# Kernel optimization log

Measured on AMD Instinct MI355X. Metric: run time of the kernel, lower is better.

## Reference

```python
import jax, jax.numpy as jnp
import numpy as np

HIDDEN = 2048
HEAD_DIM = 128
NUM_HEADS = 8
NUM_HH = 2          # num_householder
CONV = 4
EPS = 1e-5
KEY_DIM = NUM_HEADS * HEAD_DIM  # 1024


def setup_inputs() -> dict:
    key = jax.random.key(0)
    ks = jax.random.split(key, 14)
    B, L = 2, 512
    s = 0.02
    x = jax.random.normal(ks[0], (B, L, HIDDEN), jnp.float32)
    Wq = jax.random.normal(ks[1], (HIDDEN, KEY_DIM), jnp.float32) * s
    Wk = jax.random.normal(ks[2], (HIDDEN, KEY_DIM * NUM_HH), jnp.float32) * s
    Wv = jax.random.normal(ks[3], (HIDDEN, KEY_DIM * NUM_HH), jnp.float32) * s
    Wb = jax.random.normal(ks[4], (HIDDEN, NUM_HEADS * NUM_HH), jnp.float32) * s
    Wa = jax.random.normal(ks[5], (HIDDEN, NUM_HEADS), jnp.float32) * s
    A_log = jnp.log(jax.random.uniform(ks[6], (NUM_HEADS,), jnp.float32, 1e-3, 16.0))
    dt = jnp.exp(jax.random.uniform(ks[7], (NUM_HEADS,), jnp.float32)
                 * (np.float32(np.log(0.1)) - np.float32(np.log(0.001)))
                 + np.float32(np.log(0.001)))
    dt = jnp.maximum(dt, 1e-4)
    dt_bias = dt + jnp.log(-jnp.expm1(-dt))
    conv_q_w = jax.random.normal(ks[8], (KEY_DIM, 1, CONV), jnp.float32) * 0.1
    conv_k_w = jax.random.normal(ks[9], (KEY_DIM * NUM_HH, 1, CONV), jnp.float32) * 0.1
    conv_v_w = jax.random.normal(ks[10], (KEY_DIM * NUM_HH, 1, CONV), jnp.float32) * 0.1
    Wg = jax.random.normal(ks[11], (HIDDEN, KEY_DIM), jnp.float32) * s
    norm_w = jnp.ones((HEAD_DIM,), jnp.float32)
    Wo = jax.random.normal(ks[12], (KEY_DIM, HIDDEN), jnp.float32) * s
    return dict(x=x, Wq=Wq, Wk=Wk, Wv=Wv, Wb=Wb, Wa=Wa, A_log=A_log,
                dt_bias=dt_bias, conv_q_w=conv_q_w, conv_k_w=conv_k_w,
                conv_v_w=conv_v_w, Wg=Wg, norm_w=norm_w, Wo=Wo)


def _causal_conv_silu(x, w):
    # x: (B, L, C); w: (C, 1, K) depthwise causal conv, then SiLU
    y = jax.lax.conv_general_dilated(
        jnp.swapaxes(x, 1, 2), w, window_strides=(1,),
        padding=[(w.shape[-1] - 1, 0)],
        feature_group_count=w.shape[0],
        dimension_numbers=('NCH', 'OIH', 'NCH'))
    return jnp.swapaxes(jax.nn.silu(y), 1, 2)


def _l2norm(x):
    n = jnp.sqrt(jnp.sum(x * x, axis=-1, keepdims=True))
    return x / jnp.maximum(n, 1e-12)


def reference(x, Wq, Wk, Wv, Wb, Wa, A_log, dt_bias,
              conv_q_w, conv_k_w, conv_v_w, Wg, norm_w, Wo):
    B, L, _ = x.shape
    H, Dh, nh = NUM_HEADS, HEAD_DIM, NUM_HH

    q = _causal_conv_silu(x @ Wq, conv_q_w).reshape(B, L, H, Dh)
    k = _causal_conv_silu(x @ Wk, conv_k_w).reshape(B, L, nh, H, Dh)
    v = _causal_conv_silu(x @ Wv, conv_v_w).reshape(B, L, nh, H, Dh)

    q = _l2norm(q) / np.float32(np.sqrt(Dh))
    k = _l2norm(k)

    beta = 2.0 * jax.nn.sigmoid(x @ Wb).reshape(B, L, nh, H)  # allow_neg_eigval
    g = -jnp.exp(A_log) * jax.nn.softplus(x @ Wa + dt_bias)    # (B, L, H)

    def step(state, inp):
        # state: (B, H, Dh, Dh)
        q_t, k_t, v_t, b_t, g_t = inp  # (B,H,Dh),(B,nh,H,Dh),(B,nh,H,Dh),(B,nh,H),(B,H)
        state = state * jnp.exp(g_t)[..., None, None]  # gate at first sub-step
        for j in range(nh):  # Householder / delta-rule updates
            kj = k_t[:, j]
            corr = jnp.einsum('bhk,bhkv->bhv', kj, state)
            u = (v_t[:, j] - corr) * b_t[:, j][..., None]
            state = state + jnp.einsum('bhk,bhv->bhkv', kj, u)
        o_t = jnp.einsum('bhk,bhkv->bhv', q_t, state)  # readout at last sub-step
        return state, o_t

    state0 = jnp.zeros((B, H, Dh, Dh), x.dtype)
    xs = (jnp.moveaxis(q, 1, 0), jnp.moveaxis(k, 1, 0), jnp.moveaxis(v, 1, 0),
          jnp.moveaxis(beta, 1, 0), jnp.moveaxis(g, 1, 0))
    state, o = jax.lax.scan(step, state0, xs)
    o = jnp.moveaxis(o, 0, 1)  # (B, L, H, Dh)

    # gated RMSNorm: normalize o, scale by weight, gate with silu(g_proj(x))
    gate = (x @ Wg).reshape(B, L, H, Dh)
    o = o * jax.lax.rsqrt(jnp.mean(o * o, axis=-1, keepdims=True) + EPS)
    o = o * norm_w * jax.nn.silu(gate)

    out = o.reshape(B, L, H * Dh) @ Wo
    return out, state
```

## Files before the change

### kernel.cpp

```cpp
#include <hip/hip_runtime.h>
#include <hip/hip_bf16.h>
#include <cmath>

#define B_   2
#define L_   512
#define HID  2048
#define DH   128
#define NH   8
#define NHH  2
#define ROWS 1024
#define NFUSE 6144

typedef float  f32x2  __attribute__((ext_vector_type(2)));
typedef float  f32x4  __attribute__((ext_vector_type(4)));
typedef __bf16 bf16x8 __attribute__((ext_vector_type(8)));

#define AS1(p) ((const __attribute__((address_space(1))) unsigned int*)(p))
#define AS3(p) ((__attribute__((address_space(3))) unsigned int*)(p))

__device__ __forceinline__ float dpp_xor1(float x) {
  int r = __builtin_amdgcn_update_dpp(0, __float_as_int(x), 0xB1, 0xF, 0xF, true);
  return __int_as_float(r);
}
__device__ __forceinline__ float dpp_xor2(float x) {
  int r = __builtin_amdgcn_update_dpp(0, __float_as_int(x), 0x4E, 0xF, 0xF, true);
  return __int_as_float(r);
}
__device__ __forceinline__ float dpp_hmirror(float x) {
  int r = __builtin_amdgcn_update_dpp(0, __float_as_int(x), 0x141, 0xF, 0xF, true);
  return __int_as_float(r);
}
__device__ __forceinline__ float dpp_rmirror(float x) {
  int r = __builtin_amdgcn_update_dpp(0, __float_as_int(x), 0x140, 0xF, 0xF, true);
  return __int_as_float(r);
}

__global__ void f2bf_kernel(const float* __restrict__ in, __hip_bfloat16* __restrict__ out, int n) {
  int i = blockIdx.x * 256 + threadIdx.x;
  if (i < n) out[i] = __float2bfloat16(in[i]);
}

__global__ __launch_bounds__(256) void transpose5_kernel(const float* __restrict__ Wq,
                                                         const float* __restrict__ Wk,
                                                         const float* __restrict__ Wv,
                                                         const float* __restrict__ Wg,
                                                         const float* __restrict__ Wo,
                                                         __hip_bfloat16* __restrict__ WT,
                                                         __hip_bfloat16* __restrict__ WoT) {
  const float* in; __hip_bfloat16* out; int K, N;
  switch (blockIdx.z) {
    case 0: in = Wq; out = WT;                          K = 2048; N = 1024; break;
    case 1: in = Wk; out = WT + (size_t)1024 * 2048;    K = 2048; N = 2048; break;
    case 2: in = Wv; out = WT + (size_t)3072 * 2048;    K = 2048; N = 2048; break;
    case 3: in = Wg; out = WT + (size_t)5120 * 2048;    K = 2048; N = 1024; break;
    default: in = Wo; out = WoT;                        K = 1024; N = 2048; break;
  }
  __shared__ float tile[32][33];
  int n0 = blockIdx.x * 32, k0 = blockIdx.y * 32;
  if (n0 >= N || k0 >= K) return;
  int tx = threadIdx.x, ty = threadIdx.y;
#pragma unroll
  for (int i = 0; i < 32; i += 8)
    tile[ty + i][tx] = in[(size_t)(k0 + ty + i) * N + n0 + tx];
  __syncthreads();
#pragma unroll
  for (int i = 0; i < 32; i += 8)
    out[(size_t)(n0 + ty + i) * K + k0 + tx] = __float2bfloat16(tile[tx][ty + i]);
}

__global__ __launch_bounds__(256) void gemm_bf16_64(const __hip_bfloat16* __restrict__ A,
                                                    const __hip_bfloat16* __restrict__ BT,
                                                    float* __restrict__ C, int M, int N, int K) {
  __shared__ __align__(16) __hip_bfloat16 lA[64 * 32];
  __shared__ __align__(16) __hip_bfloat16 lB[128 * 32];
  const int tid = threadIdx.x;
  const int lane = tid & 63;
  const int w = tid >> 6;
  const int row0 = blockIdx.y * 64;
  const int col0 = blockIdx.x * 128;
  f32x4 acc[4][2];
#pragma unroll
  for (int m = 0; m < 4; ++m)
#pragma unroll
    for (int n = 0; n < 2; ++n) acc[m][n] = {0.f, 0.f, 0.f, 0.f};
  const int fr = lane & 15;
  const int ko = (lane >> 4) * 8;
  for (int kt = 0; kt < K; kt += 32) {
    {
      int elem = (w * 64 + lane) * 8;
      int rr = elem >> 5, cc = elem & 31;
      const __hip_bfloat16* srcA = A + (size_t)(row0 + rr) * K + kt + cc;
      __builtin_amdgcn_global_load_lds(AS1(srcA), AS3(&lA[w * 512]), 16, 0, 0);
    }
#pragma unroll
    for (int i = 0; i < 2; ++i) {
      int elem = ((i * 4 + w) * 64 + lane) * 8;
      int rr = elem >> 5, cc = elem & 31;
      const __hip_bfloat16* srcB = BT + (size_t)(col0 + rr) * K + kt + cc;
      __builtin_amdgcn_global_load_lds(AS1(srcB), AS3(&lB[(i * 4 + w) * 512]), 16, 0, 0);
    }
    __syncthreads();
    bf16x8 af[4], bfr[2];
#pragma unroll
    for (int m = 0; m < 4; ++m)
      af[m] = *reinterpret_cast<const bf16x8*>(&lA[(m * 16 + fr) * 32 + ko]);
#pragma unroll
    for (int n = 0; n < 2; ++n)
      bfr[n] = *reinterpret_cast<const bf16x8*>(&lB[(w * 32 + n * 16 + fr) * 32 + ko]);
#pragma unroll
    for (int m = 0; m < 4; ++m)
#pragma unroll
      for (int n = 0; n < 2; ++n)
        acc[m][n] = __builtin_amdgcn_mfma_f32_16x16x32_bf16(af[m], bfr[n], acc[m][n], 0, 0, 0);
    __syncthreads();
  }
  const int rq = (lane >> 4) * 4;
#pragma unroll
  for (int m = 0; m < 4; ++m)
#pragma unroll
    for (int n = 0; n < 2; ++n)
#pragma unroll
      for (int r = 0; r < 4; ++r)
        C[(size_t)(row0 + m * 16 + rq + r) * N + (col0 + w * 32 + n * 16 + fr)] =
            acc[m][n][r];
}

__device__ __forceinline__ float silu_f(float y) { return y / (1.f + __expf(-y)); }

__global__ __launch_bounds__(64) void ba_fused_kernel(const float* __restrict__ x,
                                                      const float* __restrict__ Wb,
                                                      const float* __restrict__ Wa,
                                                      const float* __restrict__ A_log,
                                                      const float* __restrict__ dt_bias,
                                                      float* __restrict__ beta_s,
                                                      float* __restrict__ ge_s) {
  const int row = blockIdx.x;
  const int lane = threadIdx.x;
  f32x4 aB0 = {0,0,0,0}, aB1 = {0,0,0,0}, aB2 = {0,0,0,0}, aB3 = {0,0,0,0};
  f32x4 aA0 = {0,0,0,0}, aA1 = {0,0,0,0};
  const float* xr = x + (size_t)row * HID;
  for (int i = 0; i < 32; ++i) {
    int k = lane + i * 64;
    float xv = xr[k];
    const f32x4* wb4 = (const f32x4*)(Wb + (size_t)k * 16);
    const f32x4* wa4 = (const f32x4*)(Wa + (size_t)k * 8);
    aB0 += wb4[0] * xv; aB1 += wb4[1] * xv; aB2 += wb4[2] * xv; aB3 += wb4[3] * xv;
    aA0 += wa4[0] * xv; aA1 += wa4[1] * xv;
  }
  __shared__ float red[64][25];
#pragma unroll
  for (int c = 0; c < 4; ++c) {
    red[lane][0 + c]  = aB0[c];
    red[lane][4 + c]  = aB1[c];
    red[lane][8 + c]  = aB2[c];
    red[lane][12 + c] = aB3[c];
    red[lane][16 + c] = aA0[c];
    red[lane][20 + c] = aA1[c];
  }
  if (lane < 24) {
    float s = 0.f;
#pragma unroll 8
    for (int i = 0; i < 64; ++i) s += red[i][lane];
    int b = row >> 9, t = row & 511;
    if (lane < 16) {
      int j = lane >> 3, h = lane & 7;
      beta_s[(((size_t)(b * 8 + h)) * 2 + j) * 512 + t] = 2.f / (1.f + __expf(-s));
    } else {
      int h = lane - 16;
      float vv = s + dt_bias[h];
      float sp = (vv > 20.f) ? vv : log1pf(__expf(vv));
      ge_s[((size_t)(b * 8 + h)) * 512 + t] = __expf(-__expf(A_log[h]) * sp);
    }
  }
}

__global__ __launch_bounds__(128) void conv_qkv_kernel(const float* __restrict__ qkvg,
                                                       const float* __restrict__ wq,
                                                       const float* __restrict__ wk,
                                                       const float* __restrict__ wv,
                                                       float* __restrict__ q_s,
                                                       float* __restrict__ k_s,
                                                       float* __restrict__ v_s) {
  int bt = blockIdx.x;
  int yy = blockIdx.y;
  int d  = threadIdx.x;
  int b = bt >> 9, t = bt & 511;
  __shared__ float red[2];
  if (yy < 8) {
    int h = yy, c = h * 128 + d;
    float y = 0.f;
#pragma unroll
    for (int tau = 0; tau < 4; ++tau) {
      int tt = t - 3 + tau;
      float xv = (tt >= 0) ? qkvg[(size_t)(b * 512 + tt) * NFUSE + c] : 0.f;
      y += xv * wq[c * 4 + tau];
    }
    y = silu_f(y);
    float ss = y * y;
#pragma unroll
    for (int off = 32; off; off >>= 1) ss += __shfl_down(ss, off);
    if ((d & 63) == 0) red[d >> 6] = ss;
    __syncthreads();
    float scale = (1.f / fmaxf(sqrtf(red[0] + red[1]), 1e-12f)) * 0.08838834764831845f;
    q_s[((size_t)(b * 8 + h) * 512 + t) * 128 + d] = y * scale;
  } else if (yy < 24) {
    int jh = yy - 8;
    int j = jh >> 3, h = jh & 7;
    int c = j * 1024 + h * 128 + d;
    float y = 0.f;
#pragma unroll
    for (int tau = 0; tau < 4; ++tau) {
      int tt = t - 3 + tau;
      float xv = (tt >= 0) ? qkvg[(size_t)(b * 512 + tt) * NFUSE + 1024 + c] : 0.f;
      y += xv * wk[c * 4 + tau];
    }
    y = silu_f(y);
    float ss = y * y;
#pragma unroll
    for (int off = 32; off; off >>= 1) ss += __shfl_down(ss, off);
    if ((d & 63) == 0) red[d >> 6] = ss;
    __syncthreads();
    float scale = 1.f / fmaxf(sqrtf(red[0] + red[1]), 1e-12f);
    k_s[(((size_t)(b * 8 + h) * 2 + j) * 512 + t) * 128 + d] = y * scale;
  } else {
    int jh = yy - 24;
    int j = jh >> 3, h = jh & 7;
    int c = j * 1024 + h * 128 + d;
    float y = 0.f;
#pragma unroll
    for (int tau = 0; tau < 4; ++tau) {
      int tt = t - 3 + tau;
      float xv = (tt >= 0) ? qkvg[(size_t)(b * 512 + tt) * NFUSE + 3072 + c] : 0.f;
      y += xv * wv[c * 4 + tau];
    }
    v_s[(((size_t)(b * 8 + h) * 2 + j) * 512 + t) * 128 + d] = silu_f(y);
  }
}

__global__ __launch_bounds__(64) void dots_kernel(const float* __restrict__ q_s,
                                                  const float* __restrict__ k_s,
                                                  float* __restrict__ dots_s) {
  const int bh = blockIdx.x;
  const int py = blockIdx.y;
  const int lane = threadIdx.x;
  const int e  = lane & 7;
  const int pl = lane >> 3;
  const int p = py * 8 + pl;
  const int tA = 2 * p;
  const float* k0A = k_s + ((size_t)bh * 2 + 0) * 512 * 128 + (size_t)tA * 128 + e * 16;
  const float* k1A = k_s + ((size_t)bh * 2 + 1) * 512 * 128 + (size_t)tA * 128 + e * 16;
  const float* qA  = q_s + (size_t)bh * 512 * 128 + (size_t)tA * 128 + e * 16;
  float d0=0,d1=0,d2=0,d3=0,d4=0,d5=0,d6=0,d7=0,d8=0,d9=0,d10=0,d11=0;
#pragma unroll
  for (int i = 0; i < 4; ++i) {
    f32x4 a0 = *(const f32x4*)(k0A + i * 4);
    f32x4 a1 = *(const f32x4*)(k1A + i * 4);
    f32x4 qa = *(const f32x4*)(qA  + i * 4);
    f32x4 b0 = *(const f32x4*)(k0A + 128 + i * 4);
    f32x4 b1 = *(const f32x4*)(k1A + 128 + i * 4);
    f32x4 qb = *(const f32x4*)(qA  + 128 + i * 4);
    f32x4 t;
#define HS(acc, u, w) t = (u) * (w); acc += (t[0] + t[1]) + (t[2] + t[3]);
    HS(d0, a1, a0) HS(d1, qa, a0) HS(d2, qa, a1)
    HS(d3, b1, b0) HS(d4, qb, b0) HS(d5, qb, b1)
    HS(d6, b0, a0) HS(d7, b0, a1) HS(d8, b1, a0) HS(d9, b1, a1)
    HS(d10, qb, a0) HS(d11, qb, a1)
#undef HS
  }
#define RED(dd) dd += dpp_xor1(dd); dd += dpp_xor2(dd); dd += dpp_hmirror(dd);
  RED(d0) RED(d1) RED(d2) RED(d3) RED(d4) RED(d5)
  RED(d6) RED(d7) RED(d8) RED(d9) RED(d10) RED(d11)
#undef RED
  if (e == 0) {
    float* dst = dots_s + (size_t)bh * 12 * 256 + p;
    dst[0*256]=d0; dst[1*256]=d1; dst[2*256]=d2;  dst[3*256]=d3;
    dst[4*256]=d4; dst[5*256]=d5; dst[6*256]=d6;  dst[7*256]=d7;
    dst[8*256]=d8; dst[9*256]=d9; dst[10*256]=d10; dst[11*256]=d11;
  }
}

#define R4(X) X(0) X(1) X(2) X(3)
#define CH 12
#define TSTEP 8
#define STEPF (3 * 16 * CH)
#define TILEF (TSTEP * STEPF)

__global__ __launch_bounds__(64, 1) void scan_kernel(const float* __restrict__ q_s,
                                                     const float* __restrict__ k_s,
                                                     const float* __restrict__ v_s,
                                                     const float* __restrict__ beta_s,
                                                     const float* __restrict__ ge_s,
                                                     const float* __restrict__ dots_s,
                                                     float* __restrict__ o_s,
                                                     float* __restrict__ state_out) {
  const int blk = blockIdx.x;
  const int bh  = blk >> 5;
  const int wg  = blk & 31;
  const int lane = threadIdx.x;
  const int kr = lane & 15;
  const int vi = lane >> 4;
  const int v  = wg * 4 + vi;

  __shared__ __align__(16) float lds[2][TILEF];
  __shared__ __align__(16) float vbuf[2][2][TSTEP][4];
  __shared__ __align__(16) float lds_sc[256][20];

  f32x4 s0 = {0.f, 0.f, 0.f, 0.f}, s1 = {0.f, 0.f, 0.f, 0.f};
#define DECLG(j) f32x4 Gk0_##j, Gk1_##j, Gq_##j;
  R4(DECLG)
#undef DECLG
  float Gv;
#define DECLSET(S) f32x4 S##_a0A,S##_a1A,S##_b0A,S##_b1A,S##_c0A,S##_c1A, \
                         S##_a0B,S##_a1B,S##_b0B,S##_b1B,S##_c0B,S##_c1B; \
  float S##_gA,S##_gB,S##_bb0A,S##_bb1A,S##_bb0B,S##_bb1B, \
        S##_d01A,S##_dq0A,S##_dq1A,S##_d01B,S##_dq0B,S##_dq1B, \
        S##_c00,S##_c01,S##_c10,S##_c11,S##_cq0,S##_cq1, \
        S##_mv0A,S##_mv1A,S##_mv0B,S##_mv1B;
  DECLSET(A) DECLSET(B)
#undef DECLSET

  const float* g_k0 = k_s + ((size_t)bh * 2 + 0) * 512 * 128;
  const float* g_k1 = k_s + ((size_t)bh * 2 + 1) * 512 * 128;
  const float* g_q  = q_s + (size_t)bh * 512 * 128;
  const float* g_v0w = v_s + ((size_t)bh * 2 + 0) * 512 * 128 + wg * 4;
  const float* g_v1w = v_s + ((size_t)bh * 2 + 1) * 512 * 128 + wg * 4;
  const float* b0p = beta_s + ((size_t)bh * 2 + 0) * 512;
  const float* b1p = beta_s + ((size_t)bh * 2 + 1) * 512;
  const float* gp  = ge_s + (size_t)bh * 512;
  const float* dp  = dots_s + (size_t)bh * 12 * 256;

#pragma unroll
  for (int i = 0; i < 4; ++i) {
    int p = lane + i * 64;
    int tA = 2 * p;
    lds_sc[p][0] = gp[tA];      lds_sc[p][1] = gp[tA + 1];
    lds_sc[p][2] = b0p[tA];     lds_sc[p][3] = b1p[tA];
    lds_sc[p][4] = b0p[tA + 1]; lds_sc[p][5] = b1p[tA + 1];
#pragma unroll
    for (int j = 0; j < 12; ++j) lds_sc[p][6 + j] = dp[j * 256 + p];
  }

  const int vhalf = lane >> 5;
  const int vli = lane & 31;
  const int vtl = vli >> 2, vc = vli & 3;
  const float* vsrc = vhalf ? g_v1w : g_v0w;

#define LD1(j) { Gk0_##j = p0[lane + j * 64]; Gk1_##j = p1[lane + j * 64]; Gq_##j = pq[lane + j * 64]; }
#define LOAD_G(T) { const f32x4* __restrict__ p0 = (const f32x4*)(g_k0 + (size_t)(T) * 1024); \
                    const f32x4* __restrict__ p1 = (const f32x4*)(g_k1 + (size_t)(T) * 1024); \
                    const f32x4* __restrict__ pq = (const f32x4*)(g_q  + (size_t)(T) * 1024); \
                    R4(LD1) }
#define LOAD_V(T) { Gv = vsrc[(size_t)(T) * 1024 + vtl * 128 + vc]; }
#define WR1(j) { int g_ = lane + 64 * j; int tl_ = g_ >> 5; int kr_ = (g_ & 31) >> 1; \
                 int c_ = 4 * (g_ & 1); \
    *(f32x4*)&lds[bsel][((tl_ * 3 + 0) * 16 + kr_) * CH + c_] = Gk0_##j; \
    *(f32x4*)&lds[bsel][((tl_ * 3 + 1) * 16 + kr_) * CH + c_] = Gk1_##j; \
    *(f32x4*)&lds[bsel][((tl_ * 3 + 2) * 16 + kr_) * CH + c_] = Gq_##j; }
#define WRITE_G(b) { const int bsel = (b); R4(WR1) }
#define WRITE_V(b) { vbuf[b][vhalf][vtl][vc] = Gv; }

#define LOAD_PAIR(S, bufx, tlx, pg) { \
    const f32x4* pk0A_ = (const f32x4*)&lds[bufx][(((tlx) * 3 + 0) * 16 + kr) * CH]; \
    const f32x4* pk1A_ = (const f32x4*)&lds[bufx][(((tlx) * 3 + 1) * 16 + kr) * CH]; \
    const f32x4* pqA_  = (const f32x4*)&lds[bufx][(((tlx) * 3 + 2) * 16 + kr) * CH]; \
    const f32x4* pk0B_ = (const f32x4*)&lds[bufx][((((tlx) + 1) * 3 + 0) * 16 + kr) * CH]; \
    const f32x4* pk1B_ = (const f32x4*)&lds[bufx][((((tlx) + 1) * 3 + 1) * 16 + kr) * CH]; \
    const f32x4* pqB_  = (const f32x4*)&lds[bufx][((((tlx) + 1) * 3 + 2) * 16 + kr) * CH]; \
    S##_a0A = pk0A_[0]; S##_a1A = pk0A_[1]; \
    S##_b0A = pk1A_[0]; S##_b1A = pk1A_[1]; \
    S##_c0A = pqA_[0];  S##_c1A = pqA_[1]; \
    S##_a0B = pk0B_[0]; S##_a1B = pk0B_[1]; \
    S##_b0B = pk1B_[0]; S##_b1B = pk1B_[1]; \
    S##_c0B = pqB_[0];  S##_c1B = pqB_[1]; \
    const f32x4* sc_ = (const f32x4*)&lds_sc[(pg) & 255][0]; \
    f32x4 y0_ = sc_[0], y1_ = sc_[1], y2_ = sc_[2], y3_ = sc_[3], y4_ = sc_[4]; \
    S##_gA = y0_[0]; S##_gB = y0_[1]; S##_bb0A = y0_[2]; S##_bb1A = y0_[3]; \
    S##_bb0B = y1_[0]; S##_bb1B = y1_[1]; S##_d01A = y1_[2]; S##_dq0A = y1_[3]; \
    S##_dq1A = y2_[0]; S##_d01B = y2_[1]; S##_dq0B = y2_[2]; S##_dq1B = y2_[3]; \
    S##_c00 = y3_[0]; S##_c01 = y3_[1]; S##_c10 = y3_[2]; S##_c11 = y3_[3]; \
    S##_cq0 = y4_[0]; S##_cq1 = y4_[1]; \
    S##_mv0A = vbuf[bufx][0][tlx][vi]; S##_mv1A = vbuf[bufx][1][tlx][vi]; \
    S##_mv0B = vbuf[bufx][0][(tlx) + 1][vi]; S##_mv1B = vbuf[bufx][1][(tlx) + 1][vi]; } \
    __builtin_amdgcn_sched_barrier(0);

#define COMPUTE_PAIR(S, pg) { \
    f32x4 r0A_ = S##_a0A * s0; r0A_ += S##_a1A * s1; \
    f32x4 r1A_ = S##_b0A * s0; r1A_ += S##_b1A * s1; \
    f32x4 rqA_ = S##_c0A * s0; rqA_ += S##_c1A * s1; \
    f32x4 r0B_ = S##_a0B * s0; r0B_ += S##_a1B * s1; \
    f32x4 r1B_ = S##_b0B * s0; r1B_ += S##_b1B * s1; \
    f32x4 rqB_ = S##_c0B * s0; rqB_ += S##_c1B * s1; \
    float h0A = (r0A_[0] + r0A_[1]) + (r0A_[2] + r0A_[3]); \
    float h1A = (r1A_[0] + r1A_[1]) + (r1A_[2] + r1A_[3]); \
    float hqA = (rqA_[0] + rqA_[1]) + (rqA_[2] + rqA_[3]); \
    float h0B = (r0B_[0] + r0B_[1]) + (r0B_[2] + r0B_[3]); \
    float h1B = (r1B_[0] + r1B_[1]) + (r1B_[2] + r1B_[3]); \
    float hqB = (rqB_[0] + rqB_[1]) + (rqB_[2] + rqB_[3]); \
    h0A += dpp_xor1(h0A); h1A += dpp_xor1(h1A); hqA += dpp_xor1(hqA); \
    h0B += dpp_xor1(h0B); h1B += dpp_xor1(h1B); hqB += dpp_xor1(hqB); \
    h0A += dpp_xor2(h0A); h1A += dpp_xor2(h1A); hqA += dpp_xor2(hqA); \
    h0B += dpp_xor2(h0B); h1B += dpp_xor2(h1B); hqB += dpp_xor2(hqB); \
    h0A += dpp_hmirror(h0A); h1A += dpp_hmirror(h1A); hqA += dpp_hmirror(hqA); \
    h0B += dpp_hmirror(h0B); h1B += dpp_hmirror(h1B); hqB += dpp_hmirror(hqB); \
    h0A += dpp_rmirror(h0A); h1A += dpp_rmirror(h1A); hqA += dpp_rmirror(hqA); \
    h0B += dpp_rmirror(h0B); h1B += dpp_rmirror(h1B); hqB += dpp_rmirror(hqB); \
    const float u0A_ = (S##_mv0A - S##_gA * h0A) * S##_bb0A; \
    const float u1A_ = (S##_mv1A - S##_gA * h1A - S##_d01A * u0A_) * S##_bb1A; \
    const float u0B_ = (S##_mv0B - S##_gB * (S##_gA * h0B + S##_c00 * u0A_ + S##_c01 * u1A_)) * S##_bb0B; \
    const float u1B_ = (S##_mv1B - S##_gB * (S##_gA * h1B + S##_c10 * u0A_ + S##_c11 * u1A_) \
                        - S##_d01B * u0B_) * S##_bb1B; \
    const float oA_ = S##_gA * hqA + S##_dq0A * u0A_ + S##_dq1A * u1A_; \
    const float oB_ = S##_gB * (S##_gA * hqB + S##_cq0 * u0A_ + S##_cq1 * u1A_) \
                      + S##_dq0B * u0B_ + S##_dq1B * u1B_; \
    const float gg_ = S##_gA * S##_gB; \
    const float w0_ = S##_gB * u0A_, w1_ = S##_gB * u1A_; \
    s0 *= gg_; s0 += S##_a0A * w0_; s0 += S##_b0A * w1_; s0 += S##_a0B * u0B_; s0 += S##_b0B * u1B_; \
    s1 *= gg_; s1 += S##_a1A * w0_; s1 += S##_b1A * w1_; s1 += S##_a1B * u0B_; s1 += S##_b1B * u1B_; \
    if (kr == 0) { const int tA_ = 2 * (pg); \
      o_s[((size_t)bh * 512 + tA_) * 128 + v] = oA_; \
      o_s[((size_t)bh * 512 + tA_ + 1) * 128 + v] = oB_; } }

  LOAD_G(0) LOAD_V(0)
  WRITE_G(0) WRITE_V(0)
  LOAD_G(1) LOAD_V(1)
  LOAD_PAIR(A, 0, 0, 0)

  for (int T = 0; T < 64; ++T) {
    const int buf = T & 1;
    if (T < 63) { WRITE_G(buf ^ 1) WRITE_V(buf ^ 1) }
    if (T < 62) { LOAD_G(T + 2) LOAD_V(T + 2) }
    const int p0i = T * 4;
    LOAD_PAIR(B, buf, 2, p0i + 1)              COMPUTE_PAIR(A, p0i + 0)
    LOAD_PAIR(A, buf, 4, p0i + 2)              COMPUTE_PAIR(B, p0i + 1)
    LOAD_PAIR(B, buf, 6, p0i + 3)              COMPUTE_PAIR(A, p0i + 2)
    LOAD_PAIR(A, buf ^ 1, 0, (p0i + 4) & 255)  COMPUTE_PAIR(B, p0i + 3)
  }

  float* base = state_out + (size_t)bh * 128 * 128 + v;
#pragma unroll
  for (int i = 0; i < 4; ++i) {
    base[(kr * 8 + i) * 128]     = s0[i];
    base[(kr * 8 + 4 + i) * 128] = s1[i];
  }
}

__global__ __launch_bounds__(128) void post_kernel(const float* __restrict__ o_s,
                                                   const float* __restrict__ qkvg,
                                                   const float* __restrict__ norm_w,
                                                   __hip_bfloat16* __restrict__ Afin) {
  int bt = blockIdx.x;
  int h = blockIdx.y;
  int d = threadIdx.x;
  int b = bt >> 9, t = bt & 511;
  int bh = b * 8 + h;
  float o = o_s[((size_t)bh * 512 + t) * 128 + d];
  __shared__ float red[2];
  float ss = o * o;
#pragma unroll
  for (int off = 32; off; off >>= 1) ss += __shfl_down(ss, off);
  if ((d & 63) == 0) red[d >> 6] = ss;
  __syncthreads();
  float mean = (red[0] + red[1]) * (1.f / 128.f);
  float r = rsqrtf(mean + 1e-5f);
  float gate = qkvg[(size_t)bt * NFUSE + 5120 + h * 128 + d];
  float val = o * r * norm_w[d] * silu_f(gate);
  Afin[(size_t)bt * 1024 + h * 128 + d] = __float2bfloat16(val);
}

extern "C" void kernel_launch(void* const* d_in, const int* in_sizes, int n_in,
                              void* d_out, int out_size, void* d_ws, size_t ws_size,
                              hipStream_t stream) {
  const float* x       = (const float*)d_in[0];
  const float* Wq      = (const float*)d_in[1];
  const float* Wk      = (const float*)d_in[2];
  const float* Wv      = (const float*)d_in[3];
  const float* Wb      = (const float*)d_in[4];
  const float* Wa      = (const float*)d_in[5];
  const float* A_log   = (const float*)d_in[6];
  const float* dt_bias = (const float*)d_in[7];
  const float* cqw     = (const float*)d_in[8];
  const float* ckw     = (const float*)d_in[9];
  const float* cvw     = (const float*)d_in[10];
  const float* Wg      = (const float*)d_in[11];
  const float* norm_w  = (const float*)d_in[12];
  const float* Wo      = (const float*)d_in[13];

  char* ws = (char*)d_ws;
  size_t off = 0;
  auto alloc = [&](size_t bytes) {
    void* p = ws + off;
    off += (bytes + 255) & ~(size_t)255;
    return p;
  };
  __hip_bfloat16* xbf  = (__hip_bfloat16*)alloc((size_t)2097152 * 2);
  __hip_bfloat16* WT   = (__hip_bfloat16*)alloc((size_t)NFUSE * 2048 * 2);
  __hip_bfloat16* WoT  = (__hip_bfloat16*)alloc((size_t)2097152 * 2);
  float* qkvg   = (float*)alloc((size_t)ROWS * NFUSE * 4);
  float* q_s    = (float*)alloc((size_t)1048576 * 4);
  float* k_s    = (float*)alloc((size_t)2097152 * 4);
  float* v_s    = (float*)alloc((size_t)2097152 * 4);
  float* beta_s = (float*)alloc((size_t)16384 * 4);
  float* ge_s   = (float*)alloc((size_t)8192 * 4);
  float* dots_s = (float*)alloc((size_t)16 * 12 * 256 * 4);
  float* o_s    = (float*)alloc((size_t)1048576 * 4);
  __hip_bfloat16* Afin = (__hip_bfloat16*)alloc((size_t)1048576 * 2);

  float* out_main  = (float*)d_out;
  float* out_state = out_main + 2097152;

  dim3 tb(32, 8);
  f2bf_kernel<<<8192, 256, 0, stream>>>(x, xbf, 2097152);
  transpose5_kernel<<<dim3(64, 64, 5), tb, 0, stream>>>(Wq, Wk, Wv, Wg, Wo, WT, WoT);

  gemm_bf16_64<<<dim3(48, 16), 256, 0, stream>>>(xbf, WT, qkvg, 1024, NFUSE, 2048);
  ba_fused_kernel<<<1024, 64, 0, stream>>>(x, Wb, Wa, A_log, dt_bias, beta_s, ge_s);

  conv_qkv_kernel<<<dim3(1024, 40), 128, 0, stream>>>(qkvg, cqw, ckw, cvw, q_s, k_s, v_s);
  dots_kernel<<<dim3(16, 32), 64, 0, stream>>>(q_s, k_s, dots_s);

  scan_kernel<<<512, 64, 0, stream>>>(q_s, k_s, v_s, beta_s, ge_s, dots_s, o_s, out_state);

  post_kernel<<<dim3(1024, 8), 128, 0, stream>>>(o_s, qkvg, norm_w, Afin);
  gemm_bf16_64<<<dim3(16, 16), 256, 0, stream>>>(Afin, WoT, out_main, 1024, 2048, 1024);
}
```

Measured before the change: 241.4 us.

## Interleave two heads per scan wave and pack scalars in dots kernel

```diff
diff --git a/kernel.cpp b/kernel.cpp
--- a/kernel.cpp
+++ b/kernel.cpp
@@ -239,7 +239,9 @@
 
 __global__ __launch_bounds__(64) void dots_kernel(const float* __restrict__ q_s,
                                                   const float* __restrict__ k_s,
-                                                  float* __restrict__ dots_s) {
+                                                  const float* __restrict__ beta_s,
+                                                  const float* __restrict__ ge_s,
+                                                  float* __restrict__ spack) {
   const int bh = blockIdx.x;
   const int py = blockIdx.y;
   const int lane = threadIdx.x;
@@ -272,124 +274,117 @@
   RED(d6) RED(d7) RED(d8) RED(d9) RED(d10) RED(d11)
 #undef RED
   if (e == 0) {
-    float* dst = dots_s + (size_t)bh * 12 * 256 + p;
-    dst[0*256]=d0; dst[1*256]=d1; dst[2*256]=d2;  dst[3*256]=d3;
-    dst[4*256]=d4; dst[5*256]=d5; dst[6*256]=d6;  dst[7*256]=d7;
-    dst[8*256]=d8; dst[9*256]=d9; dst[10*256]=d10; dst[11*256]=d11;
-  }
-}
-
-#define R4(X) X(0) X(1) X(2) X(3)
+    const float* b0p = beta_s + ((size_t)bh * 2 + 0) * 512;
+    const float* b1p = beta_s + ((size_t)bh * 2 + 1) * 512;
+    const float* gp  = ge_s + (size_t)bh * 512;
+    float* dst = spack + ((size_t)bh * 256 + p) * 20;
+    dst[0] = gp[tA];      dst[1] = gp[tA + 1];
+    dst[2] = b0p[tA];     dst[3] = b1p[tA];
+    dst[4] = b0p[tA + 1]; dst[5] = b1p[tA + 1];
+    dst[6] = d0;  dst[7] = d1;  dst[8] = d2;  dst[9] = d3;
+    dst[10] = d4; dst[11] = d5; dst[12] = d6; dst[13] = d7;
+    dst[14] = d8; dst[15] = d9; dst[16] = d10; dst[17] = d11;
+  }
+}
+
 #define CH 12
-#define TSTEP 8
-#define STEPF (3 * 16 * CH)
-#define TILEF (TSTEP * STEPF)
+#define TILEF4 (4 * 3 * 16 * CH)
 
 __global__ __launch_bounds__(64, 1) void scan_kernel(const float* __restrict__ q_s,
                                                      const float* __restrict__ k_s,
                                                      const float* __restrict__ v_s,
-                                                     const float* __restrict__ beta_s,
-                                                     const float* __restrict__ ge_s,
-                                                     const float* __restrict__ dots_s,
+                                                     const float* __restrict__ spack,
                                                      float* __restrict__ o_s,
                                                      float* __restrict__ state_out) {
   const int blk = blockIdx.x;
-  const int bh  = blk >> 5;
+  const int cp  = blk >> 5;
   const int wg  = blk & 31;
   const int lane = threadIdx.x;
   const int kr = lane & 15;
   const int vi = lane >> 4;
   const int v  = wg * 4 + vi;
-
-  __shared__ __align__(16) float lds[2][TILEF];
-  __shared__ __align__(16) float vbuf[2][2][TSTEP][4];
-  __shared__ __align__(16) float lds_sc[256][20];
-
-  f32x4 s0 = {0.f, 0.f, 0.f, 0.f}, s1 = {0.f, 0.f, 0.f, 0.f};
-#define DECLG(j) f32x4 Gk0_##j, Gk1_##j, Gq_##j;
-  R4(DECLG)
-#undef DECLG
-  float Gv;
+  const int bhX = cp * 2, bhY = cp * 2 + 1;
+
+  __shared__ __align__(16) float ldsX[2][TILEF4];
+  __shared__ __align__(16) float ldsY[2][TILEF4];
+  __shared__ __align__(16) float vbufX[2][2][4][4];
+  __shared__ __align__(16) float vbufY[2][2][4][4];
+
+  f32x4 s0X = {0,0,0,0}, s1X = {0,0,0,0};
+  f32x4 s0Y = {0,0,0,0}, s1Y = {0,0,0,0};
+  f32x4 G0X_0, G0X_1, G1X_0, G1X_1, G2X_0, G2X_1;
+  f32x4 G0Y_0, G0Y_1, G1Y_0, G1Y_1, G2Y_0, G2Y_1;
+  float GvX, GvY;
 #define DECLSET(S) f32x4 S##_a0A,S##_a1A,S##_b0A,S##_b1A,S##_c0A,S##_c1A, \
                          S##_a0B,S##_a1B,S##_b0B,S##_b1B,S##_c0B,S##_c1B; \
   float S##_gA,S##_gB,S##_bb0A,S##_bb1A,S##_bb0B,S##_bb1B, \
         S##_d01A,S##_dq0A,S##_dq1A,S##_d01B,S##_dq0B,S##_dq1B, \
         S##_c00,S##_c01,S##_c10,S##_c11,S##_cq0,S##_cq1, \
         S##_mv0A,S##_mv1A,S##_mv0B,S##_mv1B;
-  DECLSET(A) DECLSET(B)
+  DECLSET(XA) DECLSET(XB) DECLSET(YA) DECLSET(YB)
 #undef DECLSET
 
-  const float* g_k0 = k_s + ((size_t)bh * 2 + 0) * 512 * 128;
-  const float* g_k1 = k_s + ((size_t)bh * 2 + 1) * 512 * 128;
-  const float* g_q  = q_s + (size_t)bh * 512 * 128;
-  const float* g_v0w = v_s + ((size_t)bh * 2 + 0) * 512 * 128 + wg * 4;
-  const float* g_v1w = v_s + ((size_t)bh * 2 + 1) * 512 * 128 + wg * 4;
-  const float* b0p = beta_s + ((size_t)bh * 2 + 0) * 512;
-  const float* b1p = beta_s + ((size_t)bh * 2 + 1) * 512;
-  const float* gp  = ge_s + (size_t)bh * 512;
-  const float* dp  = dots_s + (size_t)bh * 12 * 256;
-
-#pragma unroll
-  for (int i = 0; i < 4; ++i) {
-    int p = lane + i * 64;
-    int tA = 2 * p;
-    lds_sc[p][0] = gp[tA];      lds_sc[p][1] = gp[tA + 1];
-    lds_sc[p][2] = b0p[tA];     lds_sc[p][3] = b1p[tA];
-    lds_sc[p][4] = b0p[tA + 1]; lds_sc[p][5] = b1p[tA + 1];
-#pragma unroll
-    for (int j = 0; j < 12; ++j) lds_sc[p][6 + j] = dp[j * 256 + p];
-  }
+  const float* g_k0X = k_s + ((size_t)bhX * 2 + 0) * 512 * 128;
+  const float* g_k1X = k_s + ((size_t)bhX * 2 + 1) * 512 * 128;
+  const float* g_qX  = q_s + (size_t)bhX * 512 * 128;
+  const float* g_k0Y = k_s + ((size_t)bhY * 2 + 0) * 512 * 128;
+  const float* g_k1Y = k_s + ((size_t)bhY * 2 + 1) * 512 * 128;
+  const float* g_qY  = q_s + (size_t)bhY * 512 * 128;
+  const float* spX = spack + (size_t)bhX * 256 * 20;
+  const float* spY = spack + (size_t)bhY * 256 * 20;
 
   const int vhalf = lane >> 5;
   const int vli = lane & 31;
-  const int vtl = vli >> 2, vc = vli & 3;
-  const float* vsrc = vhalf ? g_v1w : g_v0w;
-
-#define LD1(j) { Gk0_##j = p0[lane + j * 64]; Gk1_##j = p1[lane + j * 64]; Gq_##j = pq[lane + j * 64]; }
-#define LOAD_G(T) { const f32x4* __restrict__ p0 = (const f32x4*)(g_k0 + (size_t)(T) * 1024); \
-                    const f32x4* __restrict__ p1 = (const f32x4*)(g_k1 + (size_t)(T) * 1024); \
-                    const f32x4* __restrict__ pq = (const f32x4*)(g_q  + (size_t)(T) * 1024); \
-                    R4(LD1) }
-#define LOAD_V(T) { Gv = vsrc[(size_t)(T) * 1024 + vtl * 128 + vc]; }
-#define WR1(j) { int g_ = lane + 64 * j; int tl_ = g_ >> 5; int kr_ = (g_ & 31) >> 1; \
-                 int c_ = 4 * (g_ & 1); \
-    *(f32x4*)&lds[bsel][((tl_ * 3 + 0) * 16 + kr_) * CH + c_] = Gk0_##j; \
-    *(f32x4*)&lds[bsel][((tl_ * 3 + 1) * 16 + kr_) * CH + c_] = Gk1_##j; \
-    *(f32x4*)&lds[bsel][((tl_ * 3 + 2) * 16 + kr_) * CH + c_] = Gq_##j; }
-#define WRITE_G(b) { const int bsel = (b); R4(WR1) }
-#define WRITE_V(b) { vbuf[b][vhalf][vtl][vc] = Gv; }
-
-#define LOAD_PAIR(S, bufx, tlx, pg) { \
-    const f32x4* pk0A_ = (const f32x4*)&lds[bufx][(((tlx) * 3 + 0) * 16 + kr) * CH]; \
-    const f32x4* pk1A_ = (const f32x4*)&lds[bufx][(((tlx) * 3 + 1) * 16 + kr) * CH]; \
-    const f32x4* pqA_  = (const f32x4*)&lds[bufx][(((tlx) * 3 + 2) * 16 + kr) * CH]; \
-    const f32x4* pk0B_ = (const f32x4*)&lds[bufx][((((tlx) + 1) * 3 + 0) * 16 + kr) * CH]; \
-    const f32x4* pk1B_ = (const f32x4*)&lds[bufx][((((tlx) + 1) * 3 + 1) * 16 + kr) * CH]; \
-    const f32x4* pqB_  = (const f32x4*)&lds[bufx][((((tlx) + 1) * 3 + 2) * 16 + kr) * CH]; \
-    S##_a0A = pk0A_[0]; S##_a1A = pk0A_[1]; \
-    S##_b0A = pk1A_[0]; S##_b1A = pk1A_[1]; \
-    S##_c0A = pqA_[0];  S##_c1A = pqA_[1]; \
-    S##_a0B = pk0B_[0]; S##_a1B = pk0B_[1]; \
-    S##_b0B = pk1B_[0]; S##_b1B = pk1B_[1]; \
-    S##_c0B = pqB_[0];  S##_c1B = pqB_[1]; \
-    const f32x4* sc_ = (const f32x4*)&lds_sc[(pg) & 255][0]; \
+  const int vtlc = (vli >> 2) & 3, vc = vli & 3;
+  const float* vsrcX = v_s + ((size_t)bhX * 2 + vhalf) * 512 * 128 + wg * 4;
+  const float* vsrcY = v_s + ((size_t)bhY * 2 + vhalf) * 512 * 128 + wg * 4;
+
+#define LOAD_G(C, T) { \
+    const f32x4* p0_ = (const f32x4*)(g_k0##C + (size_t)(T) * 512); \
+    const f32x4* p1_ = (const f32x4*)(g_k1##C + (size_t)(T) * 512); \
+    const f32x4* pq_ = (const f32x4*)(g_q##C  + (size_t)(T) * 512); \
+    G0##C##_0 = p0_[lane]; G0##C##_1 = p0_[lane + 64]; \
+    G1##C##_0 = p1_[lane]; G1##C##_1 = p1_[lane + 64]; \
+    G2##C##_0 = pq_[lane]; G2##C##_1 = pq_[lane + 64]; }
+#define LOAD_V(C, T) { Gv##C = vsrc##C[((size_t)(T) * 4 + vtlc) * 128 + vc]; }
+#define WRG1(C, b, j) { int g_ = lane + 64 * (j); int tl_ = g_ >> 5; int r4_ = g_ & 31; \
+    int kr_ = r4_ >> 1; int c_ = (r4_ & 1) * 4; \
+    *(f32x4*)&lds##C[b][((tl_ * 3 + 0) * 16 + kr_) * CH + c_] = G0##C##_##j; \
+    *(f32x4*)&lds##C[b][((tl_ * 3 + 1) * 16 + kr_) * CH + c_] = G1##C##_##j; \
+    *(f32x4*)&lds##C[b][((tl_ * 3 + 2) * 16 + kr_) * CH + c_] = G2##C##_##j; }
+#define WRITE_G(C, b) { WRG1(C, b, 0) WRG1(C, b, 1) }
+#define WRITE_V(C, b) { if (vli < 16) vbuf##C[b][vhalf][vtlc][vc] = Gv##C; }
+
+#define LOAD_PAIR(CS, C, bufx, tlx, pg) { \
+    const f32x4* pk0A_ = (const f32x4*)&lds##C[bufx][(((tlx) * 3 + 0) * 16 + kr) * CH]; \
+    const f32x4* pk1A_ = (const f32x4*)&lds##C[bufx][(((tlx) * 3 + 1) * 16 + kr) * CH]; \
+    const f32x4* pqA_  = (const f32x4*)&lds##C[bufx][(((tlx) * 3 + 2) * 16 + kr) * CH]; \
+    const f32x4* pk0B_ = (const f32x4*)&lds##C[bufx][((((tlx) + 1) * 3 + 0) * 16 + kr) * CH]; \
+    const f32x4* pk1B_ = (const f32x4*)&lds##C[bufx][((((tlx) + 1) * 3 + 1) * 16 + kr) * CH]; \
+    const f32x4* pqB_  = (const f32x4*)&lds##C[bufx][((((tlx) + 1) * 3 + 2) * 16 + kr) * CH]; \
+    CS##_a0A = pk0A_[0]; CS##_a1A = pk0A_[1]; \
+    CS##_b0A = pk1A_[0]; CS##_b1A = pk1A_[1]; \
+    CS##_c0A = pqA_[0];  CS##_c1A = pqA_[1]; \
+    CS##_a0B = pk0B_[0]; CS##_a1B = pk0B_[1]; \
+    CS##_b0B = pk1B_[0]; CS##_b1B = pk1B_[1]; \
+    CS##_c0B = pqB_[0];  CS##_c1B = pqB_[1]; \
+    const f32x4* sc_ = (const f32x4*)(sp##C + (size_t)((pg) & 255) * 20); \
     f32x4 y0_ = sc_[0], y1_ = sc_[1], y2_ = sc_[2], y3_ = sc_[3], y4_ = sc_[4]; \
-    S##_gA = y0_[0]; S##_gB = y0_[1]; S##_bb0A = y0_[2]; S##_bb1A = y0_[3]; \
-    S##_bb0B = y1_[0]; S##_bb1B = y1_[1]; S##_d01A = y1_[2]; S##_dq0A = y1_[3]; \
-    S##_dq1A = y2_[0]; S##_d01B = y2_[1]; S##_dq0B = y2_[2]; S##_dq1B = y2_[3]; \
-    S##_c00 = y3_[0]; S##_c01 = y3_[1]; S##_c10 = y3_[2]; S##_c11 = y3_[3]; \
-    S##_cq0 = y4_[0]; S##_cq1 = y4_[1]; \
-    S##_mv0A = vbuf[bufx][0][tlx][vi]; S##_mv1A = vbuf[bufx][1][tlx][vi]; \
-    S##_mv0B = vbuf[bufx][0][(tlx) + 1][vi]; S##_mv1B = vbuf[bufx][1][(tlx) + 1][vi]; } \
-    __builtin_amdgcn_sched_barrier(0);
-
-#define COMPUTE_PAIR(S, pg) { \
-    f32x4 r0A_ = S##_a0A * s0; r0A_ += S##_a1A * s1; \
-    f32x4 r1A_ = S##_b0A * s0; r1A_ += S##_b1A * s1; \
-    f32x4 rqA_ = S##_c0A * s0; rqA_ += S##_c1A * s1; \
-    f32x4 r0B_ = S##_a0B * s0; r0B_ += S##_a1B * s1; \
-    f32x4 r1B_ = S##_b0B * s0; r1B_ += S##_b1B * s1; \
-    f32x4 rqB_ = S##_c0B * s0; rqB_ += S##_c1B * s1; \
+    CS##_gA = y0_[0]; CS##_gB = y0_[1]; CS##_bb0A = y0_[2]; CS##_bb1A = y0_[3]; \
+    CS##_bb0B = y1_[0]; CS##_bb1B = y1_[1]; CS##_d01A = y1_[2]; CS##_dq0A = y1_[3]; \
+    CS##_dq1A = y2_[0]; CS##_d01B = y2_[1]; CS##_dq0B = y2_[2]; CS##_dq1B = y2_[3]; \
+    CS##_c00 = y3_[0]; CS##_c01 = y3_[1]; CS##_c10 = y3_[2]; CS##_c11 = y3_[3]; \
+    CS##_cq0 = y4_[0]; CS##_cq1 = y4_[1]; \
+    CS##_mv0A = vbuf##C[bufx][0][tlx][vi]; CS##_mv1A = vbuf##C[bufx][1][tlx][vi]; \
+    CS##_mv0B = vbuf##C[bufx][0][(tlx) + 1][vi]; CS##_mv1B = vbuf##C[bufx][1][(tlx) + 1][vi]; }
+
+#define COMPUTE_PAIR(CS, C, pg) { \
+    f32x4 r0A_ = CS##_a0A * s0##C; r0A_ += CS##_a1A * s1##C; \
+    f32x4 r1A_ = CS##_b0A * s0##C; r1A_ += CS##_b1A * s1##C; \
+    f32x4 rqA_ = CS##_c0A * s0##C; rqA_ += CS##_c1A * s1##C; \
+    f32x4 r0B_ = CS##_a0B * s0##C; r0B_ += CS##_a1B * s1##C; \
+    f32x4 r1B_ = CS##_b0B * s0##C; r1B_ += CS##_b1B * s1##C; \
+    f32x4 rqB_ = CS##_c0B * s0##C; rqB_ += CS##_c1B * s1##C; \
     float h0A = (r0A_[0] + r0A_[1]) + (r0A_[2] + r0A_[3]); \
     float h1A = (r1A_[0] + r1A_[1]) + (r1A_[2] + r1A_[3]); \
     float hqA = (rqA_[0] + rqA_[1]) + (rqA_[2] + rqA_[3]); \
@@ -404,43 +399,55 @@
     h0B += dpp_hmirror(h0B); h1B += dpp_hmirror(h1B); hqB += dpp_hmirror(hqB); \
     h0A += dpp_rmirror(h0A); h1A += dpp_rmirror(h1A); hqA += dpp_rmirror(hqA); \
     h0B += dpp_rmirror(h0B); h1B += dpp_rmirror(h1B); hqB += dpp_rmirror(hqB); \
-    const float u0A_ = (S##_mv0A - S##_gA * h0A) * S##_bb0A; \
-    const float u1A_ = (S##_mv1A - S##_gA * h1A - S##_d01A * u0A_) * S##_bb1A; \
-    const float u0B_ = (S##_mv0B - S##_gB * (S##_gA * h0B + S##_c00 * u0A_ + S##_c01 * u1A_)) * S##_bb0B; \
-    const float u1B_ = (S##_mv1B - S##_gB * (S##_gA * h1B + S##_c10 * u0A_ + S##_c11 * u1A_) \
-                        - S##_d01B * u0B_) * S##_bb1B; \
-    const float oA_ = S##_gA * hqA + S##_dq0A * u0A_ + S##_dq1A * u1A_; \
-    const float oB_ = S##_gB * (S##_gA * hqB + S##_cq0 * u0A_ + S##_cq1 * u1A_) \
-                      + S##_dq0B * u0B_ + S##_dq1B * u1B_; \
-    const float gg_ = S##_gA * S##_gB; \
-    const float w0_ = S##_gB * u0A_, w1_ = S##_gB * u1A_; \
-    s0 *= gg_; s0 += S##_a0A * w0_; s0 += S##_b0A * w1_; s0 += S##_a0B * u0B_; s0 += S##_b0B * u1B_; \
-    s1 *= gg_; s1 += S##_a1A * w0_; s1 += S##_b1A * w1_; s1 += S##_a1B * u0B_; s1 += S##_b1B * u1B_; \
+    const float u0A_ = (CS##_mv0A - CS##_gA * h0A) * CS##_bb0A; \
+    const float u1A_ = (CS##_mv1A - CS##_gA * h1A - CS##_d01A * u0A_) * CS##_bb1A; \
+    const float u0B_ = (CS##_mv0B - CS##_gB * (CS##_gA * h0B + CS##_c00 * u0A_ + CS##_c01 * u1A_)) * CS##_bb0B; \
+    const float u1B_ = (CS##_mv1B - CS##_gB * (CS##_gA * h1B + CS##_c10 * u0A_ + CS##_c11 * u1A_) \
+                        - CS##_d01B * u0B_) * CS##_bb1B; \
+    const float oA_ = CS##_gA * hqA + CS##_dq0A * u0A_ + CS##_dq1A * u1A_; \
+    const float oB_ = CS##_gB * (CS##_gA * hqB + CS##_cq0 * u0A_ + CS##_cq1 * u1A_) \
+                      + CS##_dq0B * u0B_ + CS##_dq1B * u1B_; \
+    const float gg_ = CS##_gA * CS##_gB; \
+    const float w0_ = CS##_gB * u0A_, w1_ = CS##_gB * u1A_; \
+    s0##C *= gg_; s0##C += CS##_a0A * w0_; s0##C += CS##_b0A * w1_; \
+    s0##C += CS##_a0B * u0B_; s0##C += CS##_b0B * u1B_; \
+    s1##C *= gg_; s1##C += CS##_a1A * w0_; s1##C += CS##_b1A * w1_; \
+    s1##C += CS##_a1B * u0B_; s1##C += CS##_b1B * u1B_; \
     if (kr == 0) { const int tA_ = 2 * (pg); \
-      o_s[((size_t)bh * 512 + tA_) * 128 + v] = oA_; \
-      o_s[((size_t)bh * 512 + tA_ + 1) * 128 + v] = oB_; } }
-
-  LOAD_G(0) LOAD_V(0)
-  WRITE_G(0) WRITE_V(0)
-  LOAD_G(1) LOAD_V(1)
-  LOAD_PAIR(A, 0, 0, 0)
-
-  for (int T = 0; T < 64; ++T) {
+      o_s[((size_t)bh##C * 512 + tA_) * 128 + v] = oA_; \
+      o_s[((size_t)bh##C * 512 + tA_ + 1) * 128 + v] = oB_; } }
+
+  LOAD_G(X, 0) LOAD_V(X, 0) LOAD_G(Y, 0) LOAD_V(Y, 0)
+  WRITE_G(X, 0) WRITE_V(X, 0) WRITE_G(Y, 0) WRITE_V(Y, 0)
+  LOAD_G(X, 1) LOAD_V(X, 1) LOAD_G(Y, 1) LOAD_V(Y, 1)
+  LOAD_PAIR(XA, X, 0, 0, 0) LOAD_PAIR(YA, Y, 0, 0, 0)
+  __builtin_amdgcn_sched_barrier(0);
+
+  for (int T = 0; T < 128; ++T) {
     const int buf = T & 1;
-    if (T < 63) { WRITE_G(buf ^ 1) WRITE_V(buf ^ 1) }
-    if (T < 62) { LOAD_G(T + 2) LOAD_V(T + 2) }
-    const int p0i = T * 4;
-    LOAD_PAIR(B, buf, 2, p0i + 1)              COMPUTE_PAIR(A, p0i + 0)
-    LOAD_PAIR(A, buf, 4, p0i + 2)              COMPUTE_PAIR(B, p0i + 1)
-    LOAD_PAIR(B, buf, 6, p0i + 3)              COMPUTE_PAIR(A, p0i + 2)
-    LOAD_PAIR(A, buf ^ 1, 0, (p0i + 4) & 255)  COMPUTE_PAIR(B, p0i + 3)
-  }
-
-  float* base = state_out + (size_t)bh * 128 * 128 + v;
-#pragma unroll
-  for (int i = 0; i < 4; ++i) {
-    base[(kr * 8 + i) * 128]     = s0[i];
-    base[(kr * 8 + 4 + i) * 128] = s1[i];
+    if (T < 127) { WRITE_G(X, buf ^ 1) WRITE_V(X, buf ^ 1)
+                   WRITE_G(Y, buf ^ 1) WRITE_V(Y, buf ^ 1) }
+    const int p0i = T * 2;
+    LOAD_PAIR(XB, X, buf, 2, p0i + 1) LOAD_PAIR(YB, Y, buf, 2, p0i + 1)
+    __builtin_amdgcn_sched_barrier(0);
+    COMPUTE_PAIR(XA, X, p0i) COMPUTE_PAIR(YA, Y, p0i)
+    if (T < 126) { LOAD_G(X, T + 2) LOAD_V(X, T + 2)
+                   LOAD_G(Y, T + 2) LOAD_V(Y, T + 2) }
+    LOAD_PAIR(XA, X, buf ^ 1, 0, (p0i + 2) & 255) LOAD_PAIR(YA, Y, buf ^ 1, 0, (p0i + 2) & 255)
+    __builtin_amdgcn_sched_barrier(0);
+    COMPUTE_PAIR(XB, X, p0i + 1) COMPUTE_PAIR(YB, Y, p0i + 1)
+  }
+
+  {
+    float* baseX = state_out + (size_t)bhX * 128 * 128 + v;
+    float* baseY = state_out + (size_t)bhY * 128 * 128 + v;
+#pragma unroll
+    for (int i = 0; i < 4; ++i) {
+      baseX[(kr * 8 + i) * 128]     = s0X[i];
+      baseX[(kr * 8 + 4 + i) * 128] = s1X[i];
+      baseY[(kr * 8 + i) * 128]     = s0Y[i];
+      baseY[(kr * 8 + 4 + i) * 128] = s1Y[i];
+    }
   }
 }
 
@@ -501,7 +508,7 @@
   float* v_s    = (float*)alloc((size_t)2097152 * 4);
   float* beta_s = (float*)alloc((size_t)16384 * 4);
   float* ge_s   = (float*)alloc((size_t)8192 * 4);
-  float* dots_s = (float*)alloc((size_t)16 * 12 * 256 * 4);
+  float* spack  = (float*)alloc((size_t)16 * 256 * 20 * 4);
   float* o_s    = (float*)alloc((size_t)1048576 * 4);
   __hip_bfloat16* Afin = (__hip_bfloat16*)alloc((size_t)1048576 * 2);
 
@@ -516,9 +523,9 @@
   ba_fused_kernel<<<1024, 64, 0, stream>>>(x, Wb, Wa, A_log, dt_bias, beta_s, ge_s);
 
   conv_qkv_kernel<<<dim3(1024, 40), 128, 0, stream>>>(qkvg, cqw, ckw, cvw, q_s, k_s, v_s);
-  dots_kernel<<<dim3(16, 32), 64, 0, stream>>>(q_s, k_s, dots_s);
-
-  scan_kernel<<<512, 64, 0, stream>>>(q_s, k_s, v_s, beta_s, ge_s, dots_s, o_s, out_state);
+  dots_kernel<<<dim3(16, 32), 64, 0, stream>>>(q_s, k_s, beta_s, ge_s, spack);
+
+  scan_kernel<<<256, 64, 0, stream>>>(q_s, k_s, v_s, spack, o_s, out_state);
 
   post_kernel<<<dim3(1024, 8), 128, 0, stream>>>(o_s, qkvg, norm_w, Afin);
   gemm_bf16_64<<<dim3(16, 16), 256, 0, stream>>>(Afin, WoT, out_main, 1024, 2048, 1024);
```

New measurement: 376.5 us. +56.0%, slower.
